# Kernel optimization log

Hardware: AMD Instinct MI355X
Metric: run time of the kernel (lower is better)

The kernel has to match this reference:

```python
import jax, jax.numpy as jnp
import numpy as np

N = 255      # 17 joints * 15 time steps
NNZ = 2550   # ~avg degree 10
B = 512


def setup_inputs() -> dict:
    key = jax.random.key(0)
    ks = jax.random.split(key, 24)
    inp = {}
    inp["H"] = jax.random.normal(ks[0], (B, N, 2), jnp.float32)
    inp["sm_values"] = jax.random.uniform(ks[1], (NNZ,), jnp.float32)
    inp["sp_values"] = jax.random.uniform(ks[2], (NNZ,), jnp.float32)
    dims = [2, 400, 300, 100, 300, 400, 2]
    names = ["enc0", "enc1", "enc2", "dec0", "dec1", "dec2"]
    for i, nm in enumerate(names):
        din, dout = dims[i], dims[i + 1]
        inp["W_" + nm] = jax.random.normal(ks[3 + 2 * i], (din, dout), jnp.float32) * (1.0 / np.sqrt(din))
        inp["b_" + nm] = jnp.zeros((dout,), jnp.float32)
    inp["sm_indices"] = jax.random.randint(ks[20], (NNZ, 2), 0, N, dtype=jnp.int32)
    inp["sp_indices"] = jax.random.randint(ks[21], (NNZ, 2), 0, N, dtype=jnp.int32)
    return inp


def _densify(indices, values):
    # scatter sparse COO Laplacian into a tiny [N, N] dense matrix (255x255)
    return jnp.zeros((N, N), values.dtype).at[indices[:, 0], indices[:, 1]].add(values)


def reference(H, sm_values, sp_values,
              W_enc0, b_enc0, W_enc1, b_enc1, W_enc2, b_enc2,
              W_dec0, b_dec0, W_dec1, b_dec1, W_dec2, b_dec2,
              sm_indices, sp_indices):
    DADsm = _densify(sm_indices, sm_values)
    DADsp = _densify(sp_indices, sp_values)
    x = H  # [B, N, d]
    # encoder: Laplacian smoothing = ReLU(DADsm @ (x W + b)), batched over B
    for W, b in ((W_enc0, b_enc0), (W_enc1, b_enc1), (W_enc2, b_enc2)):
        x = jax.nn.relu(jnp.einsum('ij,bjd->bid', DADsm, x @ W + b))
    # decoder: Laplacian sharpening = ReLU(DADsp @ (x W + b))
    for W, b in ((W_dec0, b_dec0), (W_dec1, b_dec1), (W_dec2, b_dec2)):
        x = jax.nn.relu(jnp.einsum('ij,bjd->bid', DADsp, x @ W + b))
    return x
```

## Files before the change

### kernel.cpp

```cpp
#include <hip/hip_runtime.h>
#include <hip/hip_fp16.h>

typedef __half f16;
typedef _Float16 h8 __attribute__((ext_vector_type(8)));
typedef _Float16 h4 __attribute__((ext_vector_type(4)));
typedef _Float16 h2 __attribute__((ext_vector_type(2)));
typedef float f32x4 __attribute__((ext_vector_type(4)));

#define NN 255
#define BB 512
#define TSS 264

static __device__ __forceinline__ f16 f2h(float x) { return __float2half(x); }

union H8u { h8 v; h2 p[4]; };

__device__ __forceinline__ void conv_wt(const float* __restrict__ W, f16* __restrict__ Wtp,
                                        int K, int N, int KPB, int f, int tid) {
    int tile = f >> 6, fl = f & 63;
    int Kpad = KPB * 8;
    for (int k = tid; k < Kpad; k += 256) {
        float v = (f < N && k < K) ? W[(size_t)k * N + f] : 0.f;
        Wtp[((((size_t)tile * KPB + (k >> 3)) * 64 + fl) << 3) + (k & 7)] = f2h(v);
    }
}

__global__ __launch_bounds__(256) void setup1(
        float* __restrict__ dadsm, float* __restrict__ T5,
        const float* W1, const float* W2, const float* W3, const float* W4, const float* W5,
        f16* Wt1, f16* Wt2, f16* Wt3, f16* Wt4, f16* Wt5) {
    int bi = blockIdx.x, tid = threadIdx.x;
    if (bi < 510) { dadsm[bi * 256 + tid] = 0.f; return; }
    if (bi < 1534) { T5[(bi - 510) * 256 + tid] = 0.f; return; }
    int f = bi - 1534;
    if (f < 320) conv_wt(W1, Wt1, 400, 300, 52, f, tid);
    else if (f < 448) conv_wt(W2, Wt2, 300, 100, 40, f - 320, tid);
    else if (f < 768) conv_wt(W3, Wt3, 100, 300, 16, f - 448, tid);
    else if (f < 1216) conv_wt(W4, Wt4, 300, 400, 40, f - 768, tid);
    else conv_wt(W5, Wt5, 400, 2, 52, f - 1216, tid);
}

__global__ void setup2(const int* __restrict__ smi, const float* __restrict__ smv,
                       const int* __restrict__ spi, const float* __restrict__ spv,
                       float* __restrict__ dadsm, float* __restrict__ dadsp) {
    int t = blockIdx.x * 256 + threadIdx.x;
    if (blockIdx.x < 10) {
        if (t < 2550) atomicAdd(&dadsm[smi[2 * t] * 256 + smi[2 * t + 1]], smv[t]);
    } else {
        t -= 2560;
        if (t >= 0 && t < 2550) atomicAdd(&dadsp[spi[2 * t] * 256 + spi[2 * t + 1]], spv[t]);
    }
}

__global__ __launch_bounds__(256) void setup3(
        const float* __restrict__ dadsm, f16* __restrict__ dadpsm,
        float* __restrict__ rsm, float* __restrict__ rsp,
        const float* __restrict__ H, float* __restrict__ T0f) {
    int bi = blockIdx.x, tid = threadIdx.x;
    if (bi < 512) {
        int i = bi * 256 + tid;
        int which = i >> 16, rc = i & 65535;
        int node = rc >> 8, k = rc & 255;
        float v = (node < NN) ? dadsm[(size_t)which * NN * 256 + rc] : 0.f;
        dadpsm[(size_t)which * 65536 + (((k >> 3) * 256 + node) << 3) + (k & 7)] = f2h(v);
        return;
    }
    int lane = tid & 63;
    if (bi < 640) {
        int which = (bi < 576) ? 0 : 1;
        int base = which ? 576 : 512;
        const float* dm = dadsm + (size_t)which * NN * 256;
        float* r = which ? rsp : rsm;
        int i = (bi - base) * 4 + (tid >> 6);
        float s = 0.f;
        if (i < NN) {
            f32x4 d = ((const f32x4*)(dm + (size_t)i * 256))[lane];
            s = d.x + d.y + d.z + d.w;
#pragma unroll
            for (int off = 1; off < 64; off <<= 1) s += __shfl_xor(s, off);
        }
        if (lane == 0 && i < 256) r[i] = (i < NN) ? s : 0.f;
        return;
    }
    int gw = (bi - 640) * 4 + (tid >> 6);
    if (gw >= BB * 256) return;
    int b = gw >> 8, i = gw & 255;
    float a0 = 0.f, a1 = 0.f;
    if (i < NN) {
        f32x4 d = ((const f32x4*)(dadsm + (size_t)i * 256))[lane];
        const float2* yb2 = (const float2*)(H + (size_t)b * 510);
        float2 p0 = yb2[4 * lane], p1 = yb2[4 * lane + 1], p2 = yb2[4 * lane + 2];
        float2 p3 = (lane < 63) ? yb2[4 * lane + 3] : make_float2(0.f, 0.f);
        a0 = d.x * p0.x + d.y * p1.x + d.z * p2.x + d.w * p3.x;
        a1 = d.x * p0.y + d.y * p1.y + d.z * p2.y + d.w * p3.y;
#pragma unroll
        for (int off = 1; off < 64; off <<= 1) {
            a0 += __shfl_xor(a0, off);
            a1 += __shfl_xor(a1, off);
        }
    }
    if (lane == 0) {
        T0f[(size_t)gw * 2 + 0] = a0;
        T0f[(size_t)gw * 2 + 1] = a1;
    }
}

template <int KPB, int CT, bool R2, int MODE>
__global__ __launch_bounds__(256, 4) void fused_layer(
        const f16* __restrict__ X,
        const f16* __restrict__ Wtp,
        const float* __restrict__ bias,
        const f16* __restrict__ dadp,
        f16* __restrict__ Xn,
        int Nout, int SN, int ntiles, int rev,
        const float* __restrict__ T0p,
        const float* __restrict__ rsmp,
        const float* __restrict__ W0f,
        const float* __restrict__ b0f,
        const float* __restrict__ W5g,
        float* __restrict__ T5) {
    __shared__ _Float16 T[64 * TSS];
    __shared__ _Float16 WL[R2 ? 1344 : 4];
    const int id = blockIdx.x;
    int s = id >> 3;
    int bq = s / ntiles;
    const int tile = s - bq * ntiles;
    if (rev) bq = 63 - bq;
    const int b = ((id & 7) << 6) + bq;
    const int n0 = tile * 64;
    const int tid = threadIdx.x;
    const int w = tid >> 6;
    const int ln = tid & 15;
    const int q = (tid >> 4) & 3;

    h2 a0s[4], a1s[4], rvs[4];
    if constexpr (R2) {
        for (int i2 = tid; i2 < 448; i2 += 256) {
            WL[i2]       = (_Float16)(i2 < 400 ? W0f[i2] : 0.f);
            WL[448 + i2] = (_Float16)(i2 < 400 ? W0f[400 + i2] : 0.f);
            WL[896 + i2] = (_Float16)(i2 < 400 ? b0f[i2] : 0.f);
        }
#pragma unroll
        for (int t = 0; t < 4; t++) {
            int node = 64 * w + 16 * t + ln;
            const float* tp = T0p + ((size_t)b * 256 + node) * 2;
            _Float16 x0 = (_Float16)tp[0];
            _Float16 x1 = (_Float16)tp[1];
            _Float16 rv = (_Float16)rsmp[node];
            a0s[t] = (h2){x0, x0};
            a1s[t] = (h2){x1, x1};
            rvs[t] = (h2){rv, rv};
        }
        __syncthreads();
    }

    f32x4 acc[4][CT];
#pragma unroll
    for (int t = 0; t < 4; t++)
#pragma unroll
        for (int c = 0; c < CT; c++) acc[t][c] = (f32x4){0.f, 0.f, 0.f, 0.f};

    const f16* xb = R2 ? (const f16*)nullptr : X + (size_t)b * KPB * 2048;
    const f16* wp = Wtp + (size_t)tile * KPB * 512;

    h8 afr[2][4];
    if constexpr (!R2) {
#pragma unroll
        for (int t = 0; t < 4; t++)
            afr[0][t] = *(const h8*)(xb + ((q * 256 + 64 * w + 16 * t + ln) << 3));
    }

#pragma unroll
    for (int kb = 0; kb < KPB; kb += 4) {
        const int cur = (kb >> 2) & 1, nxt = cur ^ 1;
        h8 bf[CT];
#pragma unroll
        for (int c = 0; c < CT; c++)
            bf[c] = *(const h8*)(wp + (((kb + q) * 64 + 16 * c + ln) << 3));
        h8 afc[4];
        if constexpr (R2) {
            H8u wa, wb, bl;
            wa.v = *(const h8*)&WL[(kb + q) * 8];
            wb.v = *(const h8*)&WL[448 + (kb + q) * 8];
            bl.v = *(const h8*)&WL[896 + (kb + q) * 8];
            const h2 z2 = (h2){(_Float16)0.f, (_Float16)0.f};
#pragma unroll
            for (int t = 0; t < 4; t++) {
                H8u r;
#pragma unroll
                for (int j = 0; j < 4; j++)
                    r.p[j] = __builtin_elementwise_max(
                        a0s[t] * wa.p[j] + a1s[t] * wb.p[j] + rvs[t] * bl.p[j], z2);
                afc[t] = r.v;
            }
        } else {
            if (kb + 4 < KPB) {
#pragma unroll
                for (int t = 0; t < 4; t++)
                    afr[nxt][t] = *(const h8*)(xb + (((kb + 4 + q) * 256 + 64 * w + 16 * t + ln) << 3));
            }
#pragma unroll
            for (int t = 0; t < 4; t++) afc[t] = afr[cur][t];
        }
#pragma unroll
        for (int c = 0; c < CT; c++)
#pragma unroll
            for (int t = 0; t < 4; t++)
                acc[t][c] = __builtin_amdgcn_mfma_f32_16x16x32_f16(afc[t], bf[c], acc[t][c], 0, 0, 0);
    }

#pragma unroll
    for (int c = 0; c < CT; c++) {
        int fl = 16 * c + ln;
        int gf = n0 + fl;
        float bv = (gf < Nout) ? bias[gf] : 0.f;
#pragma unroll
        for (int t = 0; t < 4; t++) {
            h4 pk;
#pragma unroll
            for (int rg = 0; rg < 4; rg++) pk[rg] = (_Float16)(acc[t][c][rg] + bv);
            *(h4*)&T[fl * TSS + 64 * w + 16 * t + q * 4] = pk;
        }
    }
    __syncthreads();

    f32x4 acc2[CT][4];
#pragma unroll
    for (int f = 0; f < CT; f++)
#pragma unroll
        for (int t = 0; t < 4; t++) acc2[f][t] = (f32x4){0.f, 0.f, 0.f, 0.f};

    h8 b2[2][4];
#pragma unroll
    for (int t = 0; t < 4; t++)
        b2[0][t] = *(const h8*)(dadp + ((q * 256 + 64 * w + 16 * t + ln) << 3));

#pragma unroll
    for (int kb = 0; kb < 32; kb += 4) {
        const int cur = (kb >> 2) & 1, nxt = cur ^ 1;
        if (kb + 4 < 32) {
#pragma unroll
            for (int t = 0; t < 4; t++)
                b2[nxt][t] = *(const h8*)(dadp + (((kb + 4 + q) * 256 + 64 * w + 16 * t + ln) << 3));
        }
        h8 a2[CT];
#pragma unroll
        for (int f = 0; f < CT; f++)
            a2[f] = *(const h8*)&T[(16 * f + ln) * TSS + (kb + q) * 8];
#pragma unroll
        for (int t = 0; t < 4; t++)
#pragma unroll
            for (int f = 0; f < CT; f++)
                acc2[f][t] = __builtin_amdgcn_mfma_f32_16x16x32_f16(a2[f], b2[cur][t], acc2[f][t], 0, 0, 0);
    }

    if constexpr (MODE == 0) {
        f16* xn = Xn + (size_t)b * (SN >> 3) * 2048;
#pragma unroll
        for (int f = 0; f < CT; f++) {
            int fb = n0 + 16 * f + q * 4;
            if (fb >= SN) continue;
            int fb8 = fb >> 3, off = fb & 7;
#pragma unroll
            for (int t = 0; t < 4; t++) {
                int node = 64 * w + 16 * t + ln;
                h4 pk;
#pragma unroll
                for (int rg = 0; rg < 4; rg++) pk[rg] = (_Float16)fmaxf(acc2[f][t][rg], 0.f);
                *(h4*)(xn + (((size_t)fb8 * 256 + node) << 3) + off) = pk;
            }
        }
    } else {
        float s0[4], s1[4];
#pragma unroll
        for (int t = 0; t < 4; t++) { s0[t] = 0.f; s1[t] = 0.f; }
#pragma unroll
        for (int f = 0; f < CT; f++) {
#pragma unroll
            for (int rg = 0; rg < 4; rg++) {
                int feat = n0 + 16 * f + q * 4 + rg;
                float w50 = 0.f, w51 = 0.f;
                if (feat < 400) { w50 = W5g[feat * 2]; w51 = W5g[feat * 2 + 1]; }
#pragma unroll
                for (int t = 0; t < 4; t++) {
                    float v = fmaxf(acc2[f][t][rg], 0.f);
                    s0[t] += v * w50;
                    s1[t] += v * w51;
                }
            }
        }
#pragma unroll
        for (int t = 0; t < 4; t++) {
            s0[t] += __shfl_xor(s0[t], 16); s0[t] += __shfl_xor(s0[t], 32);
            s1[t] += __shfl_xor(s1[t], 16); s1[t] += __shfl_xor(s1[t], 32);
        }
        if (q == 0) {
#pragma unroll
            for (int t = 0; t < 4; t++) {
                int node = 64 * w + 16 * t + ln;
                atomicAdd(&T5[((size_t)b * 256 + node) * 2 + 0], s0[t]);
                atomicAdd(&T5[((size_t)b * 256 + node) * 2 + 1], s1[t]);
            }
        }
    }
}

__global__ __launch_bounds__(256) void dad_out(
        const float* __restrict__ dadsp, const float* __restrict__ T5,
        const float* __restrict__ rsp, const float* __restrict__ b5,
        float* __restrict__ out) {
    int gw = blockIdx.x * 4 + (threadIdx.x >> 6);
    int lane = threadIdx.x & 63;
    int b = gw >> 8, i = gw & 255;
    if (i >= NN) return;
    f32x4 d = ((const f32x4*)(dadsp + (size_t)i * 256))[lane];
    const float4* t5 = (const float4*)(T5 + (size_t)b * 512);
    float4 f0 = t5[2 * lane], f1 = t5[2 * lane + 1];
    float a0 = d.x * f0.x + d.y * f0.z + d.z * f1.x + d.w * f1.z;
    float a1 = d.x * f0.y + d.y * f0.w + d.z * f1.y + d.w * f1.w;
#pragma unroll
    for (int off = 1; off < 64; off <<= 1) {
        a0 += __shfl_xor(a0, off);
        a1 += __shfl_xor(a1, off);
    }
    if (lane == 0) {
        float rv = rsp[i];
        float2 v;
        v.x = fmaxf(a0 + rv * b5[0], 0.f);
        v.y = fmaxf(a1 + rv * b5[1], 0.f);
        *(float2*)(out + ((size_t)b * NN + i) * 2) = v;
    }
}


extern "C" void kernel_launch(void* const* d_in, const int* in_sizes, int n_in,
                              void* d_out, int out_size, void* d_ws, size_t ws_size,
                              hipStream_t stream) {
    const float* H   = (const float*)d_in[0];
    const float* W[6]  = {(const float*)d_in[3], (const float*)d_in[5], (const float*)d_in[7],
                          (const float*)d_in[9], (const float*)d_in[11], (const float*)d_in[13]};
    const float* Bv[6] = {(const float*)d_in[4], (const float*)d_in[6], (const float*)d_in[8],
                          (const float*)d_in[10], (const float*)d_in[12], (const float*)d_in[14]};
    const int* smi = (const int*)d_in[15];
    const int* spi = (const int*)d_in[16];

    char* p = (char*)d_ws;
    f16* bufA = (f16*)p;            p += 109051904;
    f16* bufB = (f16*)p;            p += 83886080;
    float* dadsm = (float*)p;       p += 261120;
    float* dadsp = (float*)p;       p += 261120;
    f16* dadpsm = (f16*)p;          p += 131072;
    f16* dadpsp = (f16*)p;          p += 131072;
    f16* Wt1 = (f16*)p;             p += 266240;
    f16* Wt2 = (f16*)p;             p += 81920;
    f16* Wt3 = (f16*)p;             p += 81920;
    f16* Wt4 = (f16*)p;             p += 286720;
    f16* Wt5 = (f16*)p;             p += 53248;
    float* T0f = (float*)p;         p += 1048576;
    float* T5  = (float*)p;         p += 1048576;
    float* rsm = (float*)p;         p += 1024;
    float* rsp = (float*)p;         p += 1024;

    setup1<<<2814, 256, 0, stream>>>(dadsm, T5, W[1], W[2], W[3], W[4], W[5],
                                     Wt1, Wt2, Wt3, Wt4, Wt5);
    setup2<<<20, 256, 0, stream>>>(smi, (const float*)d_in[1], spi, (const float*)d_in[2],
                                   dadsm, dadsp);
    setup3<<<33408, 256, 0, stream>>>(dadsm, dadpsm, rsm, rsp, H, T0f);

    fused_layer<52, 4, true,  0><<<BB * 5, 256, 0, stream>>>(
        nullptr, Wt1, Bv[1], dadpsm, bufB, 300, 320, 5, 0,
        T0f, rsm, W[0], Bv[0], nullptr, nullptr);
    fused_layer<40, 4, false, 0><<<BB * 2, 256, 0, stream>>>(
        bufB, Wt2, Bv[2], dadpsm, bufA, 100, 128, 2, 1,
        nullptr, nullptr, nullptr, nullptr, nullptr, nullptr);
    fused_layer<16, 4, false, 0><<<BB * 5, 256, 0, stream>>>(
        bufA, Wt3, Bv[3], dadpsp, bufB, 300, 320, 5, 0,
        nullptr, nullptr, nullptr, nullptr, nullptr, nullptr);
    fused_layer<40, 4, false, 2><<<BB * 7, 256, 0, stream>>>(
        bufB, Wt4, Bv[4], dadpsp, nullptr, 400, 0, 7, 1,
        nullptr, nullptr, nullptr, nullptr, W[5], T5);
    dad_out<<<32768, 256, 0, stream>>>(dadsp, T5, rsp, Bv[5], (float*)d_out);
}
```

Before: 333.1 us.

## Retile activation, weight and Laplacian buffers into 16-row MFMA fragment blocks

Changes the packed fp16 layout of activations, weights and the dense Laplacians so each 16-row fragment's K-blocks sit contiguously (16 rows x 8 halves per block), and updates all MFMA fragment loads and the inter-layer writes to match. The goal is better locality and coalescing of the per-wave fragment loads across K. Zeroing of the scatter and output accumulators moves from setup-kernel blocks to hipMemsetAsync, and the unused W5 repack is dropped. The extra memset calls add launch overhead in exchange.

```diff
diff --git a/kernel.cpp b/kernel.cpp
--- a/kernel.cpp
+++ b/kernel.cpp
@@ -15,29 +15,24 @@
 
 union H8u { h8 v; h2 p[4]; };
 
+
 __device__ __forceinline__ void conv_wt(const float* __restrict__ W, f16* __restrict__ Wtp,
                                         int K, int N, int KPB, int f, int tid) {
-    int tile = f >> 6, fl = f & 63;
     int Kpad = KPB * 8;
     for (int k = tid; k < Kpad; k += 256) {
         float v = (f < N && k < K) ? W[(size_t)k * N + f] : 0.f;
-        Wtp[((((size_t)tile * KPB + (k >> 3)) * 64 + fl) << 3) + (k & 7)] = f2h(v);
+        Wtp[((((size_t)(f >> 4) * KPB + (k >> 3)) * 16 + (f & 15)) << 3) + (k & 7)] = f2h(v);
     }
 }
 
 __global__ __launch_bounds__(256) void setup1(
-        float* __restrict__ dadsm, float* __restrict__ T5,
-        const float* W1, const float* W2, const float* W3, const float* W4, const float* W5,
-        f16* Wt1, f16* Wt2, f16* Wt3, f16* Wt4, f16* Wt5) {
-    int bi = blockIdx.x, tid = threadIdx.x;
-    if (bi < 510) { dadsm[bi * 256 + tid] = 0.f; return; }
-    if (bi < 1534) { T5[(bi - 510) * 256 + tid] = 0.f; return; }
-    int f = bi - 1534;
+        const float* W1, const float* W2, const float* W3, const float* W4,
+        f16* Wt1, f16* Wt2, f16* Wt3, f16* Wt4) {
+    int f = blockIdx.x, tid = threadIdx.x;
     if (f < 320) conv_wt(W1, Wt1, 400, 300, 52, f, tid);
     else if (f < 448) conv_wt(W2, Wt2, 300, 100, 40, f - 320, tid);
     else if (f < 768) conv_wt(W3, Wt3, 100, 300, 16, f - 448, tid);
-    else if (f < 1216) conv_wt(W4, Wt4, 300, 400, 40, f - 768, tid);
-    else conv_wt(W5, Wt5, 400, 2, 52, f - 1216, tid);
+    else conv_wt(W4, Wt4, 300, 400, 40, f - 768, tid);
 }
 
 __global__ void setup2(const int* __restrict__ smi, const float* __restrict__ smv,
@@ -62,7 +57,8 @@
         int which = i >> 16, rc = i & 65535;
         int node = rc >> 8, k = rc & 255;
         float v = (node < NN) ? dadsm[(size_t)which * NN * 256 + rc] : 0.f;
-        dadpsm[(size_t)which * 65536 + (((k >> 3) * 256 + node) << 3) + (k & 7)] = f2h(v);
+        dadpsm[(size_t)which * 65536 +
+               ((((node >> 4) * 32 + (k >> 3)) * 16 + (node & 15)) << 3) + (k & 7)] = f2h(v);
         return;
     }
     int lane = tid & 63;
@@ -167,7 +163,7 @@
     if constexpr (!R2) {
 #pragma unroll
         for (int t = 0; t < 4; t++)
-            afr[0][t] = *(const h8*)(xb + ((q * 256 + 64 * w + 16 * t + ln) << 3));
+            afr[0][t] = *(const h8*)(xb + ((((4 * w + t) * KPB + q) * 16 + ln) << 3));
     }
 
 #pragma unroll
@@ -176,7 +172,7 @@
         h8 bf[CT];
 #pragma unroll
         for (int c = 0; c < CT; c++)
-            bf[c] = *(const h8*)(wp + (((kb + q) * 64 + 16 * c + ln) << 3));
+            bf[c] = *(const h8*)(wp + (((c * KPB + kb + q) * 16 + ln) << 3));
         h8 afc[4];
         if constexpr (R2) {
             H8u wa, wb, bl;
@@ -197,7 +193,7 @@
             if (kb + 4 < KPB) {
 #pragma unroll
                 for (int t = 0; t < 4; t++)
-                    afr[nxt][t] = *(const h8*)(xb + (((kb + 4 + q) * 256 + 64 * w + 16 * t + ln) << 3));
+                    afr[nxt][t] = *(const h8*)(xb + ((((4 * w + t) * KPB + kb + 4 + q) * 16 + ln) << 3));
             }
 #pragma unroll
             for (int t = 0; t < 4; t++) afc[t] = afr[cur][t];
@@ -233,7 +229,7 @@
     h8 b2[2][4];
 #pragma unroll
     for (int t = 0; t < 4; t++)
-        b2[0][t] = *(const h8*)(dadp + ((q * 256 + 64 * w + 16 * t + ln) << 3));
+        b2[0][t] = *(const h8*)(dadp + ((((4 * w + t) * 32 + q) * 16 + ln) << 3));
 
 #pragma unroll
     for (int kb = 0; kb < 32; kb += 4) {
@@ -241,7 +237,7 @@
         if (kb + 4 < 32) {
 #pragma unroll
             for (int t = 0; t < 4; t++)
-                b2[nxt][t] = *(const h8*)(dadp + (((kb + 4 + q) * 256 + 64 * w + 16 * t + ln) << 3));
+                b2[nxt][t] = *(const h8*)(dadp + ((((4 * w + t) * 32 + kb + 4 + q) * 16 + ln) << 3));
         }
         h8 a2[CT];
 #pragma unroll
@@ -255,7 +251,8 @@
     }
 
     if constexpr (MODE == 0) {
-        f16* xn = Xn + (size_t)b * (SN >> 3) * 2048;
+        const int KPBn = SN >> 3;
+        f16* xn = Xn + (size_t)b * KPBn * 2048;
 #pragma unroll
         for (int f = 0; f < CT; f++) {
             int fb = n0 + 16 * f + q * 4;
@@ -263,11 +260,10 @@
             int fb8 = fb >> 3, off = fb & 7;
 #pragma unroll
             for (int t = 0; t < 4; t++) {
-                int node = 64 * w + 16 * t + ln;
                 h4 pk;
 #pragma unroll
                 for (int rg = 0; rg < 4; rg++) pk[rg] = (_Float16)fmaxf(acc2[f][t][rg], 0.f);
-                *(h4*)(xn + (((size_t)fb8 * 256 + node) << 3) + off) = pk;
+                *(h4*)(xn + ((((size_t)(4 * w + t) * KPBn + fb8) * 16 + ln) << 3) + off) = pk;
             }
         }
     } else {
@@ -355,14 +351,14 @@
     f16* Wt2 = (f16*)p;             p += 81920;
     f16* Wt3 = (f16*)p;             p += 81920;
     f16* Wt4 = (f16*)p;             p += 286720;
-    f16* Wt5 = (f16*)p;             p += 53248;
     float* T0f = (float*)p;         p += 1048576;
     float* T5  = (float*)p;         p += 1048576;
     float* rsm = (float*)p;         p += 1024;
     float* rsp = (float*)p;         p += 1024;
 
-    setup1<<<2814, 256, 0, stream>>>(dadsm, T5, W[1], W[2], W[3], W[4], W[5],
-                                     Wt1, Wt2, Wt3, Wt4, Wt5);
+    hipMemsetAsync(dadsm, 0, 522240, stream);
+    hipMemsetAsync(T5, 0, 1048576, stream);
+    setup1<<<1216, 256, 0, stream>>>(W[1], W[2], W[3], W[4], Wt1, Wt2, Wt3, Wt4);
     setup2<<<20, 256, 0, stream>>>(smi, (const float*)d_in[1], spi, (const float*)d_in[2],
                                    dadsm, dadsp);
     setup3<<<33408, 256, 0, stream>>>(dadsm, dadpsm, rsm, rsp, H, T0f);
```

Result: slower. 381.7 us (+14.6%).
